# Performance work log

Hardware: AMD Instinct MI355X
Metric: run time of the kernel (lower is better)

The kernel has to match this reference:

```python
import jax, jax.numpy as jnp
import numpy as np

E = 384          # embed_dim
NH = 12          # num_heads
HD = E // NH     # head_dim = 32
NC = 16          # num_clusters
SCALE = HD ** -0.5


def setup_inputs() -> dict:
    key = jax.random.key(0)
    ks = jax.random.split(key, 6)
    b, h, w = 8, 64, 64
    x = jax.random.normal(ks[0], (b, E, h, w), jnp.float32)
    qkv_w = jax.random.normal(ks[1], (3 * E, E), jnp.float32) * 0.02
    qkv_b = jnp.zeros((3 * E,), jnp.float32)
    lepe_w = jax.random.normal(ks[2], (E, 1, 5, 5), jnp.float32) * 0.02
    lepe_b = jnp.zeros((E,), jnp.float32)
    out_w = jax.random.normal(ks[3], (E, E), jnp.float32) * 0.02
    out_b = jnp.zeros((E,), jnp.float32)
    return dict(x=x, qkv_w=qkv_w, qkv_b=qkv_b, lepe_w=lepe_w,
                lepe_b=lepe_b, out_w=out_w, out_b=out_b)


def _gather_tokens(t, idx):
    # t: (b, n, l, d), idx: (b, n, l)
    return jnp.take_along_axis(t, idx[..., None], axis=2)


def reference(x, qkv_w, qkv_b, lepe_w, lepe_b, out_w, out_b):
    b, _, h, w = x.shape
    l = h * w
    lc = l // NC  # tokens per cluster

    # 1x1 conv qkv projection (channel order: [q heads | k heads | v heads])
    qkv = jnp.einsum('bchw,oc->bohw', x, qkv_w) + qkv_b[None, :, None, None]

    # lepe: 5x5 depthwise conv on the v channel slice
    v_img = qkv[:, 2 * E:]
    lepe = jax.lax.conv_general_dilated(
        v_img, lepe_w, (1, 1), ((2, 2), (2, 2)),
        feature_group_count=E,
        dimension_numbers=('NCHW', 'OIHW', 'NCHW')) + lepe_b[None, :, None, None]

    # 'b (m n d) h w -> m b n (h w) d'
    qkv = qkv.reshape(b, 3, NH, HD, l).transpose(1, 0, 2, 4, 3)  # (3,b,n,l,d)
    q, k, v = qkv[0], qkv[1], qkv[2]
    k = k * SCALE

    # cosine-similarity sort routing (sort_sim(k, k))
    cls = jnp.mean(k, axis=2, keepdims=True)                       # (b,n,1,d)
    cls = cls / jnp.maximum(jnp.linalg.norm(cls, axis=-1, keepdims=True), 1e-12)
    kn = k / jnp.maximum(jnp.linalg.norm(k, axis=-1, keepdims=True), 1e-12)
    cos = jnp.einsum('bnod,bnld->bnl', cls, kn)                    # (b,n,l)
    idx = jnp.argsort(cos, axis=-1)                                # (b,n,l)

    qs = _gather_tokens(q, idx).reshape(b, NH, NC, lc, HD)
    ks_ = _gather_tokens(k, idx).reshape(b, NH, NC, lc, HD)
    vs = _gather_tokens(v, idx).reshape(b, NH, NC, lc, HD)

    # blockwise (per-cluster) attention
    attn = jax.nn.softmax(jnp.einsum('bncld,bncmd->bnclm', qs, ks_), axis=-1)
    o = jnp.einsum('bnclm,bncmd->bncld', attn, vs).reshape(b, NH, l, HD)

    # restore original token order (inverse permutation)
    inv = jnp.argsort(idx, axis=-1)
    o = _gather_tokens(o, inv)

    # 'b n (h w) d -> b (n d) h w'
    o = o.transpose(0, 1, 3, 2).reshape(b, E, h, w)

    res = o + lepe
    return jnp.einsum('bchw,oc->bohw', res, out_w) + out_b[None, :, None, None]
```

## Files before the change

### kernel.cpp

```cpp
#include <hip/hip_runtime.h>
#include <math.h>

#define SCALE_F   0.17677669529663687f
#define SCALE_L2E 0.25505837072959003f

using bf16x8 = __attribute__((ext_vector_type(8))) __bf16;
using f32x2  = __attribute__((ext_vector_type(2))) float;
using f32x4  = __attribute__((ext_vector_type(4))) float;
using f32x16 = __attribute__((ext_vector_type(16))) float;
using uint2e = __attribute__((ext_vector_type(2))) unsigned int;

__device__ inline unsigned short f2bf(float x) {
    __bf16 h = (__bf16)x;
    return __builtin_bit_cast(unsigned short, h);
}
__device__ inline float bf2f(unsigned short u) {
    unsigned int x = ((unsigned int)u) << 16;
    return __builtin_bit_cast(float, x);
}
__device__ inline unsigned int packbf(float a, float b) {
    return (unsigned int)f2bf(a) | ((unsigned int)f2bf(b) << 16);
}
__device__ inline bf16x8 ldfrag(const unsigned short* p) {
    return __builtin_bit_cast(bf16x8, *reinterpret_cast<const uint4*>(p));
}

__global__ __launch_bounds__(512)
void gemm_k_kernel(const float* __restrict__ A, const float* __restrict__ Bmat,
                   const float* __restrict__ bias, float* __restrict__ CT)
{
    const int bm = blockIdx.x, bn = blockIdx.y, bz = blockIdx.z;
    const float* Bp = Bmat + (long)bz * 384 * 4096;
    float* Cp = CT + (long)bz * 4096 * 384;
    __shared__ float As[32][132];
    __shared__ float BsF[32 * 136];
    const int tid = threadIdx.x;
    const int tx = tid & 15, ty = tid >> 4;
    const int m0 = bm * 128, n0 = bn * 128;

    f32x2 acc2[4][4];
    #pragma unroll
    for (int i = 0; i < 4; ++i)
        #pragma unroll
        for (int p = 0; p < 4; ++p) acc2[i][p] = (f32x2){0.f, 0.f};

    for (int k0 = 0; k0 < 384; k0 += 32) {
        if (k0) __syncthreads();
        #pragma unroll
        for (int it = 0; it < 2; ++it) {
            int slot = tid + it * 512;
            int rA = slot >> 3, cA = slot & 7;
            float4 av = *reinterpret_cast<const float4*>(&A[(long)(384 + m0 + rA) * 384 + k0 + cA * 4]);
            As[cA * 4 + 0][rA] = av.x; As[cA * 4 + 1][rA] = av.y;
            As[cA * 4 + 2][rA] = av.z; As[cA * 4 + 3][rA] = av.w;
            int sr = slot >> 5, sq = slot & 31;
            int wB = sr * 136 + ((sq & 1) << 6) + ((sq >> 1) << 2);
            *reinterpret_cast<float4*>(&BsF[wB]) =
                *reinterpret_cast<const float4*>(&Bp[(long)(k0 + sr) * 4096 + n0 + sq * 4]);
        }
        __syncthreads();
        #pragma unroll
        for (int kk = 0; kk < 32; ++kk) {
            float a[4];
            *reinterpret_cast<float4*>(&a[0]) = *reinterpret_cast<const float4*>(&As[kk][ty * 4]);
            float4 blo = *reinterpret_cast<const float4*>(&BsF[kk * 136 + tx * 4]);
            float4 bhi = *reinterpret_cast<const float4*>(&BsF[kk * 136 + 64 + tx * 4]);
            f32x2 b2[4];
            b2[0] = (f32x2){blo.x, blo.y}; b2[1] = (f32x2){blo.z, blo.w};
            b2[2] = (f32x2){bhi.x, bhi.y}; b2[3] = (f32x2){bhi.z, bhi.w};
            #pragma unroll
            for (int i = 0; i < 4; ++i) {
                f32x2 a2 = (f32x2){a[i], a[i]};
                #pragma unroll
                for (int p = 0; p < 4; ++p)
                    acc2[i][p] = __builtin_elementwise_fma(a2, b2[p], acc2[i][p]);
            }
        }
    }

    float bv[4];
    #pragma unroll
    for (int i = 0; i < 4; ++i) bv[i] = bias[384 + m0 + ty * 4 + i];
    #pragma unroll
    for (int p = 0; p < 4; ++p)
        #pragma unroll
        for (int c = 0; c < 2; ++c) {
            int j = 2 * p + c;
            long tok = n0 + tx * 8 + j;
            float4 v = make_float4(acc2[0][p][c] + bv[0], acc2[1][p][c] + bv[1],
                                   acc2[2][p][c] + bv[2], acc2[3][p][c] + bv[3]);
            *reinterpret_cast<float4*>(Cp + tok * 384 + m0 + ty * 4) = v;
        }
}

template<bool SPLIT, int SM>
__global__ __launch_bounds__(256)
void mfma_nt_kernel(const unsigned short* __restrict__ Ah, const unsigned short* __restrict__ Al,
                    const unsigned short* __restrict__ Bh, const unsigned short* __restrict__ Bl,
                    const float* __restrict__ bias, void* __restrict__ Cout,
                    int K, int lda, int ldb,
                    long strideAb, long strideBb, long strideCb)
{
    extern __shared__ unsigned short smem[];
    unsigned short* As  = smem;
    unsigned short* Bs  = smem + 5120;
    unsigned short* Asl = smem + 10240;
    unsigned short* Bsl = smem + 15360;
    const int bm = blockIdx.x, bn = blockIdx.y, bz = blockIdx.z;
    const unsigned short* Ap = Ah + (long)bz * strideAb;
    const unsigned short* Bp = Bh + (long)bz * strideBb;
    const unsigned short* Alp = nullptr;
    const unsigned short* Blp = nullptr;
    if constexpr (SPLIT) {
        Alp = Al + (long)bz * strideAb;
        Blp = Bl + (long)bz * strideBb;
    }
    const int tid = threadIdx.x;
    const int lane = tid & 63, wid = tid >> 6;
    const int wr = wid >> 1, wc = wid & 1;
    const int l15 = lane & 15, l4 = lane >> 4;
    const int m0 = bm * 128, n0 = bn * 128;

    const f32x4 Z4 = {0.f, 0.f, 0.f, 0.f};
    f32x4 acc[4][4];
    #pragma unroll
    for (int i = 0; i < 4; ++i)
        #pragma unroll
        for (int j = 0; j < 4; ++j) acc[i][j] = Z4;

    for (int k0 = 0; k0 < K; k0 += 32) {
        if (k0) __syncthreads();
        #pragma unroll
        for (int it = 0; it < 2; ++it) {
            int slot = tid + it * 256;
            int r = slot >> 2, cq = slot & 3;
            *reinterpret_cast<uint4*>(&As[r * 40 + cq * 8]) =
                *reinterpret_cast<const uint4*>(&Ap[(long)(m0 + r) * lda + k0 + cq * 8]);
            *reinterpret_cast<uint4*>(&Bs[r * 40 + cq * 8]) =
                *reinterpret_cast<const uint4*>(&Bp[(long)(n0 + r) * ldb + k0 + cq * 8]);
            if constexpr (SPLIT) {
                *reinterpret_cast<uint4*>(&Asl[r * 40 + cq * 8]) =
                    *reinterpret_cast<const uint4*>(&Alp[(long)(m0 + r) * lda + k0 + cq * 8]);
                *reinterpret_cast<uint4*>(&Bsl[r * 40 + cq * 8]) =
                    *reinterpret_cast<const uint4*>(&Blp[(long)(n0 + r) * ldb + k0 + cq * 8]);
            }
        }
        __syncthreads();

        bf16x8 af[4], bg[4], afl[4], bgl[4];
        #pragma unroll
        for (int f = 0; f < 4; ++f) {
            af[f] = ldfrag(&As[(wr * 64 + f * 16 + l15) * 40 + l4 * 8]);
            bg[f] = ldfrag(&Bs[(wc * 64 + f * 16 + l15) * 40 + l4 * 8]);
        }
        if constexpr (SPLIT) {
            #pragma unroll
            for (int f = 0; f < 4; ++f) {
                afl[f] = ldfrag(&Asl[(wr * 64 + f * 16 + l15) * 40 + l4 * 8]);
                bgl[f] = ldfrag(&Bsl[(wc * 64 + f * 16 + l15) * 40 + l4 * 8]);
            }
        }
        #pragma unroll
        for (int fi = 0; fi < 4; ++fi)
            #pragma unroll
            for (int fj = 0; fj < 4; ++fj) {
                acc[fi][fj] = __builtin_amdgcn_mfma_f32_16x16x32_bf16(af[fi], bg[fj], acc[fi][fj], 0, 0, 0);
                if constexpr (SPLIT) {
                    acc[fi][fj] = __builtin_amdgcn_mfma_f32_16x16x32_bf16(af[fi], bgl[fj], acc[fi][fj], 0, 0, 0);
                    acc[fi][fj] = __builtin_amdgcn_mfma_f32_16x16x32_bf16(afl[fi], bg[fj], acc[fi][fj], 0, 0, 0);
                }
            }
    }

    if constexpr (SM == 0) {
        unsigned short* Cq = (unsigned short*)Cout + (long)bz * strideCb;
        #pragma unroll
        for (int fi = 0; fi < 4; ++fi)
            #pragma unroll
            for (int fj = 0; fj < 4; ++fj) {
                const int m = m0 + wr * 64 + fi * 16 + l4 * 4;
                const int t = n0 + wc * 64 + fj * 16 + l15;
                ushort4 h;
                h.x = f2bf(acc[fi][fj][0] + bias[m + 0]);
                h.y = f2bf(acc[fi][fj][1] + bias[m + 1]);
                h.z = f2bf(acc[fi][fj][2] + bias[m + 2]);
                h.w = f2bf(acc[fi][fj][3] + bias[m + 3]);
                *reinterpret_cast<ushort4*>(&Cq[(long)t * 768 + m]) = h;
            }
    } else {
        float* Cf = (float*)Cout + (long)bz * strideCb;
        #pragma unroll
        for (int fi = 0; fi < 4; ++fi)
            #pragma unroll
            for (int fj = 0; fj < 4; ++fj) {
                const int t = m0 + wr * 64 + fi * 16 + l4 * 4;
                const int m = n0 + wc * 64 + fj * 16 + l15;
                const float bv = bias[m];
                float4 v = make_float4(acc[fi][fj][0] + bv, acc[fi][fj][1] + bv,
                                       acc[fi][fj][2] + bv, acc[fi][fj][3] + bv);
                *reinterpret_cast<float4*>(&Cf[(long)m * 4096 + t]) = v;
            }
    }
}

__global__ __launch_bounds__(256)
void convert_w_kernel(const float* __restrict__ qkv_w, const float* __restrict__ qkv_b,
                      const float* __restrict__ out_w,
                      unsigned short* __restrict__ Wqv, float* __restrict__ qvb,
                      unsigned short* __restrict__ owh, unsigned short* __restrict__ owl)
{
    const int total = 294912 + 147456 + 768;
    for (int i = blockIdx.x * 256 + threadIdx.x; i < total; i += gridDim.x * 256) {
        if (i < 294912) {
            int m = i / 384, k = i - m * 384;
            int src = (m < 384) ? m : m + 384;
            Wqv[i] = f2bf(qkv_w[(long)src * 384 + k]);
        } else if (i < 294912 + 147456) {
            int o = i - 294912;
            float w = out_w[o];
            unsigned short h = f2bf(w);
            owh[o] = h;
            owl[o] = f2bf(w - bf2f(h));
        } else {
            int m = i - 294912 - 147456;
            qvb[m] = qkv_b[(m < 384) ? m : m + 384];
        }
    }
}

__global__ __launch_bounds__(256)
void transpose_x_kernel(const float* __restrict__ x, unsigned short* __restrict__ xbT)
{
    const int t0 = blockIdx.x * 64, c0 = blockIdx.y * 64, b = blockIdx.z;
    __shared__ float tl[64][65];
    const int tid = threadIdx.x;
    #pragma unroll
    for (int i = 0; i < 16; ++i) {
        int cr = (tid >> 6) + i * 4, tc = tid & 63;
        tl[cr][tc] = x[((long)b * 384 + c0 + cr) * 4096 + t0 + tc];
    }
    __syncthreads();
    #pragma unroll
    for (int i = 0; i < 8; ++i) {
        int tr = (tid >> 5) + i * 8, c2 = (tid & 31) * 2;
        unsigned int u = packbf(tl[c2][tr], tl[c2 + 1][tr]);
        *reinterpret_cast<unsigned int*>(&xbT[((long)b * 4096 + t0 + tr) * 384 + c0 + c2]) = u;
    }
}

__global__ __launch_bounds__(256)
void lepe_kernel(const unsigned short* __restrict__ qvB, const float* __restrict__ w5,
                 const float* __restrict__ wb, unsigned short* __restrict__ lepeT)
{
    const int ch0 = blockIdx.x * 16;
    const int y0 = blockIdx.y * 8;
    const int b = blockIdx.z;
    const unsigned short* vb = qvB + (long)b * 4096 * 768 + 384 + ch0;
    unsigned short* dst = lepeT + (long)b * 4096 * 384 + ch0;
    __shared__ float tile[12 * 68 * 16];
    const int tid = threadIdx.x;

    for (int i = tid; i < 12 * 68 * 16; i += 256) {
        int pix = i >> 4, c = i & 15;
        int yy = pix / 68, xx = pix % 68;
        int gy = y0 + yy - 2, gx = xx - 2;
        float v = 0.f;
        if (gy >= 0 && gy < 64 && gx >= 0 && gx < 64)
            v = bf2f(vb[(long)(gy * 64 + gx) * 768 + c]);
        tile[i] = v;
    }
    const int c = tid & 15, xo = tid >> 4;
    float f[25];
    #pragma unroll
    for (int j = 0; j < 25; ++j) f[j] = w5[(ch0 + c) * 25 + j];
    const float bv = wb[ch0 + c];
    __syncthreads();

    #pragma unroll
    for (int yy = 0; yy < 8; ++yy) {
        #pragma unroll
        for (int xq = 0; xq < 4; ++xq) {
            int x = xq * 16 + xo;
            float acc = bv;
            #pragma unroll
            for (int dy = 0; dy < 5; ++dy)
                #pragma unroll
                for (int dx = 0; dx < 5; ++dx)
                    acc += tile[((yy + dy) * 68 + (x + dx)) * 16 + c] * f[dy * 5 + dx];
            dst[(long)((y0 + yy) * 64 + x) * 384 + c] = f2bf(acc);
        }
    }
}

__global__ __launch_bounds__(256)
void cos_kernel(const float* __restrict__ Kf32, float* __restrict__ cosv)
{
    const int bn = blockIdx.x;
    const int b = bn / 12, n = bn % 12;
    const float* kb = Kf32 + (long)b * 4096 * 384 + n * 32;
    __shared__ float part[256][33];
    __shared__ float clsn[32];
    const int tid = threadIdx.x;
    float acc[32];
    #pragma unroll
    for (int d = 0; d < 32; ++d) acc[d] = 0.f;
    for (int i = 0; i < 16; ++i) {
        long tok = tid + i * 256;
        const float* kr = kb + tok * 384;
        #pragma unroll
        for (int d = 0; d < 32; ++d) acc[d] += kr[d];
    }
    #pragma unroll
    for (int d = 0; d < 32; ++d) part[tid][d] = acc[d];
    __syncthreads();
    if (tid < 32) {
        double s = 0.0;
        for (int t = 0; t < 256; ++t) s += (double)part[t][tid];
        part[0][tid] = (float)s;
    }
    __syncthreads();
    if (tid == 0) {
        double nn = 0.0;
        for (int d = 0; d < 32; ++d) { double v = (double)part[0][d]; nn += v * v; }
        double inv = 1.0 / sqrt(nn > 1e-300 ? nn : 1e-300);
        for (int d = 0; d < 32; ++d) clsn[d] = (float)((double)part[0][d] * inv);
    }
    __syncthreads();
    for (int i = 0; i < 16; ++i) {
        long tok = tid + i * 256;
        const float* kr = kb + tok * 384;
        double dot = 0.0, nrm = 0.0;
        #pragma unroll
        for (int d = 0; d < 32; ++d) {
            float kv = kr[d];
            dot += (double)clsn[d] * (double)kv;
            nrm += (double)kv * (double)kv;
        }
        double cv = dot / sqrt(nrm > 1e-300 ? nrm : 1e-300);
        cosv[(long)bn * 4096 + tok] = (float)cv;
    }
}

__global__ __launch_bounds__(1024)
void sort_kernel(const float* __restrict__ cosv, int* __restrict__ idxo)
{
    const int bn = blockIdx.x;
    __shared__ float sv[4096];
    __shared__ int si[4096];
    const int tid = threadIdx.x;
    for (int i = tid; i < 4096; i += 1024) { sv[i] = cosv[(long)bn * 4096 + i]; si[i] = i; }
    __syncthreads();
    for (int size = 2; size <= 4096; size <<= 1) {
        for (int stride = size >> 1; stride >= 1; stride >>= 1) {
            #pragma unroll 2
            for (int i = tid; i < 2048; i += 1024) {
                int lo = (i << 1) - (i & (stride - 1));
                int hi = lo + stride;
                bool asc = ((lo & size) == 0);
                float av = sv[lo], bvv = sv[hi];
                int ai = si[lo], bi = si[hi];
                bool agtb = (av > bvv) || (av == bvv && ai > bi);
                if (agtb == asc) {
                    sv[lo] = bvv; sv[hi] = av;
                    si[lo] = bi; si[hi] = ai;
                }
            }
            __syncthreads();
        }
    }
    for (int i = tid; i < 4096; i += 1024) idxo[(long)bn * 4096 + i] = si[i];
}

__global__ __launch_bounds__(256)
void attn_kernel(const float* __restrict__ Kf32, unsigned short* __restrict__ qvB,
                 const int* __restrict__ idxbuf, const unsigned short* __restrict__ lepeT)
{
    const int cc = blockIdx.x, n = blockIdx.y, b = blockIdx.z;
    const int* ip = idxbuf + ((long)(b * 12 + n)) * 4096 + cc * 256;

    __shared__ unsigned short KsL[256][36];
    __shared__ unsigned short VsT[32][260];
    __shared__ int tokLds[256];

    const int tid = threadIdx.x;
    const int w = tid >> 6;
    const int lane = tid & 63;
    const int lo5 = lane & 31;
    const int hi = lane >> 5;
    const int hi8 = hi * 8;

    const int tk0 = ip[tid];
    tokLds[tid] = tk0;
    const long tb = (long)b * 4096 + tk0;
    const unsigned short* qrow = qvB + tb * 768 + n * 32;
    const float* krow = Kf32 + tb * 384 + n * 32;

    unsigned int Pq[16];
    #pragma unroll
    for (int i = 0; i < 4; ++i) {
        uint4 qu = *reinterpret_cast<const uint4*>(qrow + i * 8);
        Pq[4 * i + 0] = qu.x; Pq[4 * i + 1] = qu.y;
        Pq[4 * i + 2] = qu.z; Pq[4 * i + 3] = qu.w;
    }
    #pragma unroll
    for (int dq = 0; dq < 8; ++dq) {
        float4 kv = *reinterpret_cast<const float4*>(krow + dq * 4);
        ushort4 kp;
        kp.x = f2bf(kv.x * SCALE_L2E); kp.y = f2bf(kv.y * SCALE_L2E);
        kp.z = f2bf(kv.z * SCALE_L2E); kp.w = f2bf(kv.w * SCALE_L2E);
        *reinterpret_cast<ushort4*>(&KsL[tid][dq * 4]) = kp;
    }
    {
        union { uint4 u[4]; unsigned short s[32]; } vv;
        const unsigned short* vrow = qrow + 384;
        #pragma unroll
        for (int i = 0; i < 4; ++i) vv.u[i] = *reinterpret_cast<const uint4*>(vrow + i * 8);
        #pragma unroll
        for (int j = 0; j < 32; ++j) VsT[j][tid] = vv.s[j];
    }

    bf16x8 qf00, qf01, qf10, qf11;
    {
        unsigned int w0[2][4], w1[2][4];
        #pragma unroll
        for (int ks = 0; ks < 2; ++ks)
            #pragma unroll
            for (int j = 0; j < 4; ++j) {
                uint2e r = __builtin_amdgcn_permlane32_swap(Pq[ks * 8 + j], Pq[ks * 8 + 4 + j], false, false);
                w0[ks][j] = r[0];
                w1[ks][j] = r[1];
            }
        qf00 = __builtin_bit_cast(bf16x8, make_uint4(w0[0][0], w0[0][1], w0[0][2], w0[0][3]));
        qf01 = __builtin_bit_cast(bf16x8, make_uint4(w0[1][0], w0[1][1], w0[1][2], w0[1][3]));
        qf10 = __builtin_bit_cast(bf16x8, make_uint4(w1[0][0], w1[0][1], w1[0][2], w1[0][3]));
        qf11 = __builtin_bit_cast(bf16x8, make_uint4(w1[1][0], w1[1][1], w1[1][2], w1[1][3]));
    }
    __syncthreads();

    const f32x16 Z16 = {0,0,0,0,0,0,0,0,0,0,0,0,0,0,0,0};
    f32x16 o0 = Z16, o1 = Z16;
    float lsum0 = 0.f, lsum1 = 0.f;

#define LDFRAG(ARR, ROW, OFF) ({ \
    const unsigned short* _p = &ARR[ROW][OFF]; \
    union { bf16x8 v; ushort4 h[2]; } _u; \
    _u.h[0] = *reinterpret_cast<const ushort4*>(_p); \
    _u.h[1] = *reinterpret_cast<const ushort4*>(_p + 4); \
    _u.v; })

#define EXP16(S, LS) { _Pragma("unroll") for (int r = 0; r < 16; ++r) { float _e = __builtin_exp2f(S[r]); S[r] = _e; LS += _e; } }

#define MKPB(S, H) ({ \
    unsigned int _x0 = packbf(S[(H) * 8 + 0], S[(H) * 8 + 1]); \
    unsigned int _x1 = packbf(S[(H) * 8 + 2], S[(H) * 8 + 3]); \
    unsigned int _x2 = packbf(S[(H) * 8 + 4], S[(H) * 8 + 5]); \
    unsigned int _x3 = packbf(S[(H) * 8 + 6], S[(H) * 8 + 7]); \
    uint2e _r02 = __builtin_amdgcn_permlane32_swap(_x0, _x2, false, false); \
    uint2e _r13 = __builtin_amdgcn_permlane32_swap(_x1, _x3, false, false); \
    __builtin_bit_cast(bf16x8, make_uint4(_r02[0], _r13[0], _r02[1], _r13[1])); })

    for (int ch = 0; ch < 4; ++ch) {
        const int rb = ch * 64;
        f32x16 s00 = Z16, s01 = Z16, s10 = Z16, s11 = Z16;
        bf16x8 ka;
        ka = LDFRAG(KsL, rb + lo5, hi8);
        s00 = __builtin_amdgcn_mfma_f32_32x32x16_bf16(ka, qf00, s00, 0, 0, 0);
        s01 = __builtin_amdgcn_mfma_f32_32x32x16_bf16(ka, qf10, s01, 0, 0, 0);
        ka = LDFRAG(KsL, rb + lo5, 16 + hi8);
        s00 = __builtin_amdgcn_mfma_f32_32x32x16_bf16(ka, qf01, s00, 0, 0, 0);
        s01 = __builtin_amdgcn_mfma_f32_32x32x16_bf16(ka, qf11, s01, 0, 0, 0);
        ka = LDFRAG(KsL, rb + 32 + lo5, hi8);
        s10 = __builtin_amdgcn_mfma_f32_32x32x16_bf16(ka, qf00, s10, 0, 0, 0);
        s11 = __builtin_amdgcn_mfma_f32_32x32x16_bf16(ka, qf10, s11, 0, 0, 0);
        ka = LDFRAG(KsL, rb + 32 + lo5, 16 + hi8);
        s10 = __builtin_amdgcn_mfma_f32_32x32x16_bf16(ka, qf01, s10, 0, 0, 0);
        s11 = __builtin_amdgcn_mfma_f32_32x32x16_bf16(ka, qf11, s11, 0, 0, 0);

        EXP16(s00, lsum0); EXP16(s01, lsum1);
        EXP16(s10, lsum0); EXP16(s11, lsum1);

        bf16x8 va, pb0, pb1;
        va = LDFRAG(VsT, lo5, rb + 0 + hi8);
        pb0 = MKPB(s00, 0); pb1 = MKPB(s01, 0);
        o0 = __builtin_amdgcn_mfma_f32_32x32x16_bf16(va, pb0, o0, 0, 0, 0);
        o1 = __builtin_amdgcn_mfma_f32_32x32x16_bf16(va, pb1, o1, 0, 0, 0);
        va = LDFRAG(VsT, lo5, rb + 16 + hi8);
        pb0 = MKPB(s00, 1); pb1 = MKPB(s01, 1);
        o0 = __builtin_amdgcn_mfma_f32_32x32x16_bf16(va, pb0, o0, 0, 0, 0);
        o1 = __builtin_amdgcn_mfma_f32_32x32x16_bf16(va, pb1, o1, 0, 0, 0);
        va = LDFRAG(VsT, lo5, rb + 32 + hi8);
        pb0 = MKPB(s10, 0); pb1 = MKPB(s11, 0);
        o0 = __builtin_amdgcn_mfma_f32_32x32x16_bf16(va, pb0, o0, 0, 0, 0);
        o1 = __builtin_amdgcn_mfma_f32_32x32x16_bf16(va, pb1, o1, 0, 0, 0);
        va = LDFRAG(VsT, lo5, rb + 48 + hi8);
        pb0 = MKPB(s10, 1); pb1 = MKPB(s11, 1);
        o0 = __builtin_amdgcn_mfma_f32_32x32x16_bf16(va, pb0, o0, 0, 0, 0);
        o1 = __builtin_amdgcn_mfma_f32_32x32x16_bf16(va, pb1, o1, 0, 0, 0);
    }

    const float lf0 = lsum0 + __shfl_xor(lsum0, 32);
    const float lf1 = lsum1 + __shfl_xor(lsum1, 32);
    const float li0 = 1.f / lf0, li1 = 1.f / lf1;

    #pragma unroll
    for (int qt = 0; qt < 2; ++qt) {
        const int qrix = w * 64 + qt * 32 + lo5;
        const int tk = tokLds[qrix];
        const long tb2 = (long)b * 4096 + tk;
        unsigned short* resrow = qvB + tb2 * 768;
        const unsigned short* lp = lepeT + tb2 * 384 + n * 32;
        const float li = qt ? li1 : li0;
        const f32x16& oo = qt ? o1 : o0;
        #pragma unroll
        for (int qd = 0; qd < 4; ++qd) {
            const int d0 = qd * 8 + hi * 4;
            ushort4 lv = *reinterpret_cast<const ushort4*>(lp + d0);
            float r0 = oo[qd * 4 + 0] * li + bf2f(lv.x);
            float r1 = oo[qd * 4 + 1] * li + bf2f(lv.y);
            float r2 = oo[qd * 4 + 2] * li + bf2f(lv.z);
            float r3 = oo[qd * 4 + 3] * li + bf2f(lv.w);
            unsigned short h0 = f2bf(r0), h1 = f2bf(r1), h2 = f2bf(r2), h3 = f2bf(r3);
            ushort4 hh = {h0, h1, h2, h3};
            ushort4 ll = {f2bf(r0 - bf2f(h0)), f2bf(r1 - bf2f(h1)),
                          f2bf(r2 - bf2f(h2)), f2bf(r3 - bf2f(h3))};
            *reinterpret_cast<ushort4*>(resrow + n * 32 + d0) = hh;
            *reinterpret_cast<ushort4*>(resrow + 384 + n * 32 + d0) = ll;
        }
    }
#undef LDFRAG
#undef EXP16
#undef MKPB
}

extern "C" void kernel_launch(void* const* d_in, const int* in_sizes, int n_in,
                              void* d_out, int out_size, void* d_ws, size_t ws_size,
                              hipStream_t stream)
{
    const float* x      = (const float*)d_in[0];
    const float* qkv_w  = (const float*)d_in[1];
    const float* qkv_b  = (const float*)d_in[2];
    const float* lepe_w = (const float*)d_in[3];
    const float* lepe_b = (const float*)d_in[4];
    const float* out_w  = (const float*)d_in[5];
    const float* out_b  = (const float*)d_in[6];
    float* out = (float*)d_out;

    char* ws = (char*)d_ws;
    float*          Kf32 = (float*)ws;
    unsigned short* qvB  = (unsigned short*)(ws + 50331648);
    float*          cosv = (float*)(ws + 100663296);
    int*            idx  = (int*)(ws + 102236160);
    unsigned short* Wqv  = (unsigned short*)(ws + 103809024);
    unsigned short* owh  = (unsigned short*)(ws + 104398848);
    unsigned short* owl  = (unsigned short*)(ws + 104693760);
    float*          qvb  = (float*)(ws + 104988672);

    unsigned short* xbT   = (unsigned short*)d_out;
    unsigned short* lepeT = (unsigned short*)d_out + 12582912;

    convert_w_kernel<<<1731, 256, 0, stream>>>(qkv_w, qkv_b, out_w, Wqv, qvb, owh, owl);
    transpose_x_kernel<<<dim3(64, 6, 8), 256, 0, stream>>>(x, xbT);
    gemm_k_kernel<<<dim3(3, 32, 8), 512, 0, stream>>>(qkv_w, x, qkv_b, Kf32);
    mfma_nt_kernel<false, 0><<<dim3(6, 32, 8), 256, 20480, stream>>>(
        Wqv, nullptr, xbT, nullptr, qvb, qvB,
        384, 384, 384, 0L, (long)4096 * 384, (long)4096 * 768);
    lepe_kernel<<<dim3(24, 8, 8), 256, 0, stream>>>(qvB, lepe_w, lepe_b, lepeT);
    cos_kernel<<<96, 256, 0, stream>>>(Kf32, cosv);
    sort_kernel<<<96, 1024, 0, stream>>>(cosv, idx);
    attn_kernel<<<dim3(16, 12, 8), 256, 0, stream>>>(Kf32, qvB, idx, lepeT);
    mfma_nt_kernel<true, 1><<<dim3(32, 3, 8), 256, 40960, stream>>>(
        qvB, qvB + 384, owh, owl, out_b, out,
        384, 768, 384, (long)4096 * 768, 0L, (long)384 * 4096);
}
```

Baseline: 448.6 us.

## Split cosine kernel, pack sort keys, vectorize lepe loads, prioritize MFMA

```diff
diff --git a/kernel.cpp b/kernel.cpp
--- a/kernel.cpp
+++ b/kernel.cpp
@@ -260,14 +260,21 @@
     __shared__ float tile[12 * 68 * 16];
     const int tid = threadIdx.x;
 
-    for (int i = tid; i < 12 * 68 * 16; i += 256) {
-        int pix = i >> 4, c = i & 15;
+    for (int s = tid; s < 12 * 68 * 2; s += 256) {
+        int pix = s >> 1, half = s & 1;
         int yy = pix / 68, xx = pix % 68;
         int gy = y0 + yy - 2, gx = xx - 2;
-        float v = 0.f;
-        if (gy >= 0 && gy < 64 && gx >= 0 && gx < 64)
-            v = bf2f(vb[(long)(gy * 64 + gx) * 768 + c]);
-        tile[i] = v;
+        float* tp = &tile[pix * 16 + half * 8];
+        if (gy >= 0 && gy < 64 && gx >= 0 && gx < 64) {
+            uint4 u = *reinterpret_cast<const uint4*>(vb + (long)(gy * 64 + gx) * 768 + half * 8);
+            tp[0] = bf2f((unsigned short)(u.x & 0xFFFFu)); tp[1] = bf2f((unsigned short)(u.x >> 16));
+            tp[2] = bf2f((unsigned short)(u.y & 0xFFFFu)); tp[3] = bf2f((unsigned short)(u.y >> 16));
+            tp[4] = bf2f((unsigned short)(u.z & 0xFFFFu)); tp[5] = bf2f((unsigned short)(u.z >> 16));
+            tp[6] = bf2f((unsigned short)(u.w & 0xFFFFu)); tp[7] = bf2f((unsigned short)(u.w >> 16));
+        } else {
+            #pragma unroll
+            for (int j = 0; j < 8; ++j) tp[j] = 0.f;
+        }
     }
     const int c = tid & 15, xo = tid >> 4;
     float f[25];
@@ -293,13 +300,12 @@
 }
 
 __global__ __launch_bounds__(256)
-void cos_kernel(const float* __restrict__ Kf32, float* __restrict__ cosv)
+void cls_kernel(const float* __restrict__ Kf32, float* __restrict__ clsg)
 {
     const int bn = blockIdx.x;
     const int b = bn / 12, n = bn % 12;
     const float* kb = Kf32 + (long)b * 4096 * 384 + n * 32;
     __shared__ float part[256][33];
-    __shared__ float clsn[32];
     const int tid = threadIdx.x;
     float acc[32];
     #pragma unroll
@@ -323,11 +329,25 @@
         double nn = 0.0;
         for (int d = 0; d < 32; ++d) { double v = (double)part[0][d]; nn += v * v; }
         double inv = 1.0 / sqrt(nn > 1e-300 ? nn : 1e-300);
-        for (int d = 0; d < 32; ++d) clsn[d] = (float)((double)part[0][d] * inv);
-    }
-    __syncthreads();
-    for (int i = 0; i < 16; ++i) {
-        long tok = tid + i * 256;
+        for (int d = 0; d < 32; ++d) clsg[bn * 32 + d] = (float)((double)part[0][d] * inv);
+    }
+}
+
+__global__ __launch_bounds__(256)
+void cos2_kernel(const float* __restrict__ Kf32, const float* __restrict__ clsg,
+                 float* __restrict__ cosv)
+{
+    const int bn = blockIdx.x;
+    const int b = bn / 12, n = bn % 12;
+    const float* kb = Kf32 + (long)b * 4096 * 384 + n * 32;
+    const int t0 = blockIdx.y * 512;
+    const int tid = threadIdx.x;
+    float clsn[32];
+    #pragma unroll
+    for (int d = 0; d < 32; ++d) clsn[d] = clsg[bn * 32 + d];
+    #pragma unroll
+    for (int i = 0; i < 2; ++i) {
+        long tok = t0 + tid + i * 256;
         const float* kr = kb + tok * 384;
         double dot = 0.0, nrm = 0.0;
         #pragma unroll
@@ -345,10 +365,13 @@
 void sort_kernel(const float* __restrict__ cosv, int* __restrict__ idxo)
 {
     const int bn = blockIdx.x;
-    __shared__ float sv[4096];
-    __shared__ int si[4096];
-    const int tid = threadIdx.x;
-    for (int i = tid; i < 4096; i += 1024) { sv[i] = cosv[(long)bn * 4096 + i]; si[i] = i; }
+    __shared__ unsigned long long sk[4096];
+    const int tid = threadIdx.x;
+    for (int i = tid; i < 4096; i += 1024) {
+        unsigned int u = __builtin_bit_cast(unsigned int, cosv[(long)bn * 4096 + i]);
+        u = (u & 0x80000000u) ? ~u : (u | 0x80000000u);
+        sk[i] = ((unsigned long long)u << 32) | (unsigned int)i;
+    }
     __syncthreads();
     for (int size = 2; size <= 4096; size <<= 1) {
         for (int stride = size >> 1; stride >= 1; stride >>= 1) {
@@ -357,18 +380,14 @@
                 int lo = (i << 1) - (i & (stride - 1));
                 int hi = lo + stride;
                 bool asc = ((lo & size) == 0);
-                float av = sv[lo], bvv = sv[hi];
-                int ai = si[lo], bi = si[hi];
-                bool agtb = (av > bvv) || (av == bvv && ai > bi);
-                if (agtb == asc) {
-                    sv[lo] = bvv; sv[hi] = av;
-                    si[lo] = bi; si[hi] = ai;
-                }
+                unsigned long long a = sk[lo], bq = sk[hi];
+                if ((a > bq) == asc) { sk[lo] = bq; sk[hi] = a; }
             }
             __syncthreads();
         }
     }
-    for (int i = tid; i < 4096; i += 1024) idxo[(long)bn * 4096 + i] = si[i];
+    for (int i = tid; i < 4096; i += 1024)
+        idxo[(long)bn * 4096 + i] = (int)(sk[i] & 0xFFFFFFFFu);
 }
 
 __global__ __launch_bounds__(256)
@@ -463,6 +482,7 @@
         const int rb = ch * 64;
         f32x16 s00 = Z16, s01 = Z16, s10 = Z16, s11 = Z16;
         bf16x8 ka;
+        __builtin_amdgcn_s_setprio(1);
         ka = LDFRAG(KsL, rb + lo5, hi8);
         s00 = __builtin_amdgcn_mfma_f32_32x32x16_bf16(ka, qf00, s00, 0, 0, 0);
         s01 = __builtin_amdgcn_mfma_f32_32x32x16_bf16(ka, qf10, s01, 0, 0, 0);
@@ -475,11 +495,13 @@
         ka = LDFRAG(KsL, rb + 32 + lo5, 16 + hi8);
         s10 = __builtin_amdgcn_mfma_f32_32x32x16_bf16(ka, qf01, s10, 0, 0, 0);
         s11 = __builtin_amdgcn_mfma_f32_32x32x16_bf16(ka, qf11, s11, 0, 0, 0);
+        __builtin_amdgcn_s_setprio(0);
 
         EXP16(s00, lsum0); EXP16(s01, lsum1);
         EXP16(s10, lsum0); EXP16(s11, lsum1);
 
         bf16x8 va, pb0, pb1;
+        __builtin_amdgcn_s_setprio(1);
         va = LDFRAG(VsT, lo5, rb + 0 + hi8);
         pb0 = MKPB(s00, 0); pb1 = MKPB(s01, 0);
         o0 = __builtin_amdgcn_mfma_f32_32x32x16_bf16(va, pb0, o0, 0, 0, 0);
@@ -496,6 +518,7 @@
         pb0 = MKPB(s10, 1); pb1 = MKPB(s11, 1);
         o0 = __builtin_amdgcn_mfma_f32_32x32x16_bf16(va, pb0, o0, 0, 0, 0);
         o1 = __builtin_amdgcn_mfma_f32_32x32x16_bf16(va, pb1, o1, 0, 0, 0);
+        __builtin_amdgcn_s_setprio(0);
     }
 
     const float lf0 = lsum0 + __shfl_xor(lsum0, 32);
@@ -554,6 +577,7 @@
     unsigned short* owh  = (unsigned short*)(ws + 104398848);
     unsigned short* owl  = (unsigned short*)(ws + 104693760);
     float*          qvb  = (float*)(ws + 104988672);
+    float*          clsg = (float*)(ws + 104991744);
 
     unsigned short* xbT   = (unsigned short*)d_out;
     unsigned short* lepeT = (unsigned short*)d_out + 12582912;
@@ -565,7 +589,8 @@
         Wqv, nullptr, xbT, nullptr, qvb, qvB,
         384, 384, 384, 0L, (long)4096 * 384, (long)4096 * 768);
     lepe_kernel<<<dim3(24, 8, 8), 256, 0, stream>>>(qvB, lepe_w, lepe_b, lepeT);
-    cos_kernel<<<96, 256, 0, stream>>>(Kf32, cosv);
+    cls_kernel<<<96, 256, 0, stream>>>(Kf32, clsg);
+    cos2_kernel<<<dim3(96, 8), 256, 0, stream>>>(Kf32, clsg, cosv);
     sort_kernel<<<96, 1024, 0, stream>>>(cosv, idx);
     attn_kernel<<<dim3(16, 12, 8), 256, 0, stream>>>(Kf32, qvB, idx, lepeT);
     mfma_nt_kernel<true, 1><<<dim3(32, 3, 8), 256, 40960, stream>>>(
```

Result: faster. 401.3 us (-10.6%).
